# Optimization experiments

Measured on AMD Instinct MI355X. Metric: run time of the kernel, lower is better.

The kernel has to match this reference:

```python
import jax, jax.numpy as jnp
import numpy as np

B, S_ENC, S_DEC, ENC_H, DEC_H = 8, 2048, 2048, 512, 512


def setup_inputs() -> dict:
    key = jax.random.key(0)
    k1, k2, k3 = jax.random.split(key, 3)
    return {
        "enc_hidden_states": jax.random.normal(k1, (B, S_ENC, ENC_H), dtype=jnp.float32),
        "dec_hidden_states": jax.random.normal(k2, (B, S_DEC, DEC_H), dtype=jnp.float32),
        "W_att": jax.random.normal(k3, (ENC_H, DEC_H), dtype=jnp.float32),
    }


def reference(enc_hidden_states, dec_hidden_states, W_att):
    # Project encoder states: [B, S_enc, dec_h]
    enc_proj = jnp.einsum("bse,ed->bsd", enc_hidden_states, W_att)
    # Luong 'general' scores for all decoder timesteps at once: [B, S_dec, S_enc]
    # (original code loops over decoder timesteps via tf.map_fn; this is the
    # equivalent single batched matmul)
    att_logits = jnp.einsum("btd,bsd->bts", dec_hidden_states, enc_proj)
    att_softmax = jax.nn.softmax(att_logits, axis=-1)
    # Attention context vectors: [B, S_dec, enc_h]
    att_vector = jnp.einsum("bts,bse->bte", att_softmax, enc_hidden_states)
    return att_vector
```

## Files before the change

### kernel.cpp

```cpp
#include <hip/hip_runtime.h>
#include <cstdint>


#define DEVINL __device__ __forceinline__

typedef __attribute__((ext_vector_type(8))) short short8;
typedef __attribute__((ext_vector_type(4))) float f32x4;

DEVINL short f2bf(float x) {
    union { float f; uint32_t u; } v; v.f = x;
    uint32_t r = v.u + 0x7FFFu + ((v.u >> 16) & 1u);
    return (short)(r >> 16);
}
DEVINL float bf2f(short h) {
    union { uint32_t u; float f; } v; v.u = ((uint32_t)(uint16_t)h) << 16;
    return v.f;
}

DEVINL void gload_lds16(const void* g, void* l) {
    __builtin_amdgcn_global_load_lds(
        (const __attribute__((address_space(1))) char*)g,
        (__attribute__((address_space(3))) char*)l, 16, 0, 0);
}

__global__ __launch_bounds__(256)
void split_kernel(const float* __restrict__ x, short* __restrict__ hi,
                  short* __restrict__ lo)
{
    long i = ((long)blockIdx.x * 256 + threadIdx.x) * 8;
    f32x4 a = *(const f32x4*)(x + i);
    f32x4 b = *(const f32x4*)(x + i + 4);
    short8 h, l;
#pragma unroll
    for (int j = 0; j < 4; j++) {
        short ha = f2bf(a[j]); h[j] = ha;     l[j] = f2bf(a[j] - bf2f(ha));
        short hb = f2bf(b[j]); h[4 + j] = hb; l[4 + j] = f2bf(b[j] - bf2f(hb));
    }
    *(short8*)(hi + i) = h;
    *(short8*)(lo + i) = l;
}

__global__ __launch_bounds__(256)
void split_w_kernel(const float* __restrict__ w, short* __restrict__ wth,
                    short* __restrict__ wtl)
{
    int idx = blockIdx.x * 256 + threadIdx.x;
    int k = idx >> 9, n = idx & 511;
    float v = w[idx];
    short h = f2bf(v);
    wth[(long)n * 512 + k] = h;
    wtl[(long)n * 512 + k] = f2bf(v - bf2f(h));
}

__global__ __launch_bounds__(256)
void transpose_bf16_kernel(const float* __restrict__ x, short* __restrict__ xt)
{
    __shared__ short tile[32][33];
    const int b  = blockIdx.z;
    const int s0 = blockIdx.x * 32;
    const int e0 = blockIdx.y * 32;
    const float* px = x + (long)b * 2048 * 512;
    short* pt = xt + (long)b * 512 * 2048;
    const int tx = threadIdx.x & 31;
    const int ty = threadIdx.x >> 5;
#pragma unroll
    for (int r = 0; r < 32; r += 8)
        tile[ty + r][tx] = f2bf(px[(long)(s0 + ty + r) * 512 + e0 + tx]);
    __syncthreads();
#pragma unroll
    for (int r = 0; r < 32; r += 8)
        pt[(long)(e0 + ty + r) * 2048 + s0 + tx] = tile[tx][ty + r];
}

template<int NTERMS, bool SPLIT_OUT>
__global__ __launch_bounds__(256, 2)
void gemm_bt(const short* __restrict__ Ah, const short* __restrict__ Al,
             const short* __restrict__ Bh, const short* __restrict__ Bl,
             float* __restrict__ C, short* __restrict__ Ch, short* __restrict__ Cl,
             int K, int lda, int ldb, int ldc,
             long sA, long sB, long sC)
{
    extern __shared__ char smem_raw[];
    constexpr int OPS = (NTERMS == 3) ? 4 : 2;
    constexpr int SET = 128 * 32 * OPS;
    short* smem = (short*)smem_raw;

    const int tid  = threadIdx.x;
    const int wave = tid >> 6;
    const int lane = tid & 63;
    const int quad = lane >> 4;
    const int l16  = lane & 15;
    const int wm   = (wave >> 1) * 64;
    const int wn   = (wave & 1) * 64;

    const long tile_m = (long)blockIdx.y * 128;
    const long tile_n = (long)blockIdx.x * 128;
    const int  bz     = blockIdx.z;

    const short* pAh = Ah + (long)bz * sA;
    const short* pBh = Bh + (long)bz * sB;
    const short* pAl = (NTERMS == 3) ? (Al + (long)bz * sA) : nullptr;
    const short* pBl = (NTERMS == 3) ? (Bl + (long)bz * sB) : nullptr;

    const int srow = tid >> 2;
    const int skq  = (tid & 3) * 8;
    const int lds_off = srow * 32 + skq;
    const long ga0 = (tile_m + srow) * (long)lda + skq;
    const long gb0 = (tile_n + srow) * (long)ldb + skq;

    auto stage = [&](int k0, int buf) {
        short* s   = smem + buf * SET;
        short* ash = s;
        short* bsh = s + 128 * 32;
        gload_lds16(pAh + ga0 + k0,             ash + lds_off);
        gload_lds16(pAh + ga0 + 64l * lda + k0, ash + lds_off + 64 * 32);
        gload_lds16(pBh + gb0 + k0,             bsh + lds_off);
        gload_lds16(pBh + gb0 + 64l * ldb + k0, bsh + lds_off + 64 * 32);
        if constexpr (NTERMS == 3) {
            short* asl = s + 2 * 128 * 32;
            short* bsl = s + 3 * 128 * 32;
            gload_lds16(pAl + ga0 + k0,             asl + lds_off);
            gload_lds16(pAl + ga0 + 64l * lda + k0, asl + lds_off + 64 * 32);
            gload_lds16(pBl + gb0 + k0,             bsl + lds_off);
            gload_lds16(pBl + gb0 + 64l * ldb + k0, bsl + lds_off + 64 * 32);
        }
    };

    f32x4 acc[4][4] = {};
    stage(0, 0);
    int cur = 0;

    for (int k0 = 0; k0 < K; k0 += 32) {
        __syncthreads();
        if (k0 + 32 < K) stage(k0 + 32, cur ^ 1);

        short* s   = smem + cur * SET;
        short* ash = s;
        short* bsh = s + 128 * 32;
        short* asl = s + 2 * 128 * 32;
        short* bsl = s + 3 * 128 * 32;

        short8 ah[4], bh[4], al[4], bl[4];
#pragma unroll
        for (int i = 0; i < 4; i++) {
            ah[i] = *(const short8*)&ash[(wm + i * 16 + l16) * 32 + quad * 8];
            bh[i] = *(const short8*)&bsh[(wn + i * 16 + l16) * 32 + quad * 8];
            if constexpr (NTERMS == 3) {
                al[i] = *(const short8*)&asl[(wm + i * 16 + l16) * 32 + quad * 8];
                bl[i] = *(const short8*)&bsl[(wn + i * 16 + l16) * 32 + quad * 8];
            }
        }
#pragma unroll
        for (int i = 0; i < 4; i++)
#pragma unroll
            for (int j = 0; j < 4; j++) {
                acc[i][j] = __builtin_amdgcn_mfma_f32_16x16x32_bf16(ah[i], bh[j], acc[i][j], 0, 0, 0);
                if constexpr (NTERMS == 3) {
                    acc[i][j] = __builtin_amdgcn_mfma_f32_16x16x32_bf16(ah[i], bl[j], acc[i][j], 0, 0, 0);
                    acc[i][j] = __builtin_amdgcn_mfma_f32_16x16x32_bf16(al[i], bh[j], acc[i][j], 0, 0, 0);
                }
            }
        cur ^= 1;
    }

#pragma unroll
    for (int i = 0; i < 4; i++)
#pragma unroll
        for (int j = 0; j < 4; j++) {
            const long row0 = tile_m + wm + i * 16 + quad * 4;
            const long col  = tile_n + wn + j * 16 + l16;
#pragma unroll
            for (int r = 0; r < 4; r++) {
                float v = acc[i][j][r];
                if constexpr (SPLIT_OUT) {
                    long idx = (long)bz * sC + (row0 + r) * (long)ldc + col;
                    short h = f2bf(v);
                    Ch[idx] = h;
                    Cl[idx] = f2bf(v - bf2f(h));
                } else {
                    C[(long)bz * sC + (row0 + r) * (long)ldc + col] = v;
                }
            }
        }
}

__global__ __launch_bounds__(512, 2)
void gemm3_256(const short* __restrict__ Ah, const short* __restrict__ Al,
               const short* __restrict__ Bh, const short* __restrict__ Bl,
               float* __restrict__ C,
               int K, int lda, int ldb, int ldc,
               long sA, long sB, long sC, int nbx, int nby)
{
    extern __shared__ char smem_raw[];
    short* smem = (short*)smem_raw;
    constexpr int PL  = 256 * 32;
    constexpr int SET = 4 * PL;

    const int t    = threadIdx.x;
    const int wave = t >> 6;
    const int lane = t & 63;
    const int quad = lane >> 4;
    const int l16  = lane & 15;
    const int wm   = (wave >> 2) * 128;
    const int wn   = (wave & 3) * 64;
    const int kslot8 = ((quad ^ ((l16 >> 1) & 3)) << 3);

    const int nwg = gridDim.x;
    const int wg  = blockIdx.x;
    const int swz = (wg & 7) * (nwg >> 3) + (wg >> 3);
    const int per_b = nbx * nby;
    const int bz  = swz / per_b;
    const int rem = swz - bz * per_b;
    const long tile_m = (long)(rem / nbx) * 256;
    const long tile_n = (long)(rem % nbx) * 256;

    const short* pAh = Ah + (long)bz * sA;
    const short* pAl = Al + (long)bz * sA;
    const short* pBh = Bh + (long)bz * sB;
    const short* pBl = Bl + (long)bz * sB;

    const int srow   = t >> 2;
    const int schunk = (t & 3) ^ ((t >> 3) & 3);
    const long gA  = (tile_m + srow) * (long)lda + schunk * 8;
    const long gB  = (tile_n + srow) * (long)ldb + schunk * 8;
    const long gA2 = gA + 128l * lda;
    const long gB2 = gB + 128l * ldb;
    const int ld0 = t * 8;

    f32x4 acc[8][4] = {};

    {
        short* s = smem;
        gload_lds16(pAh + gA,  s + ld0);
        gload_lds16(pAh + gA2, s + ld0 + 4096);
        gload_lds16(pBh + gB,  s + 2 * PL + ld0);
        gload_lds16(pBh + gB2, s + 2 * PL + ld0 + 4096);
        gload_lds16(pAl + gA,  s + PL + ld0);
        gload_lds16(pAl + gA2, s + PL + ld0 + 4096);
        gload_lds16(pBl + gB,  s + 3 * PL + ld0);
        gload_lds16(pBl + gB2, s + 3 * PL + ld0 + 4096);
    }
    asm volatile("s_waitcnt vmcnt(4)" ::: "memory");
    __builtin_amdgcn_s_barrier();

    const int NT = K >> 5;
    int cur = 0;
#pragma unroll 1
    for (int kt = 0; kt < NT; ++kt) {
        const short* s  = smem + cur * SET;
        short* sn       = smem + (cur ^ 1) * SET;
        const short* ah_p = s;
        const short* al_p = s + PL;
        const short* bh_p = s + 2 * PL;
        const short* bl_p = s + 3 * PL;
        const int  k0n  = (kt + 1) << 5;
        const bool more = (kt + 1 < NT);

        short8 xa[8], xb[4];

#pragma unroll
        for (int i = 0; i < 8; i++)
            xa[i] = *(const short8*)&ah_p[(wm + i * 16 + l16) * 32 + kslot8];
#pragma unroll
        for (int j = 0; j < 4; j++)
            xb[j] = *(const short8*)&bh_p[(wn + j * 16 + l16) * 32 + kslot8];
        if (more) {
            gload_lds16(pAh + gA  + k0n, sn + ld0);
            gload_lds16(pAh + gA2 + k0n, sn + ld0 + 4096);
            gload_lds16(pBh + gB  + k0n, sn + 2 * PL + ld0);
            gload_lds16(pBh + gB2 + k0n, sn + 2 * PL + ld0 + 4096);
            asm volatile("s_waitcnt vmcnt(6)" ::: "memory");
        } else {
            asm volatile("s_waitcnt vmcnt(2)" ::: "memory");
        }
        __builtin_amdgcn_s_barrier();
        asm volatile("s_waitcnt lgkmcnt(0)" ::: "memory");
        __builtin_amdgcn_s_setprio(1);
#pragma unroll
        for (int i = 0; i < 8; i++)
#pragma unroll
            for (int j = 0; j < 4; j++)
                acc[i][j] = __builtin_amdgcn_mfma_f32_16x16x32_bf16(xa[i], xb[j], acc[i][j], 0, 0, 0);
        __builtin_amdgcn_s_setprio(0);
        __builtin_amdgcn_s_barrier();

#pragma unroll
        for (int i = 0; i < 8; i++)
            xa[i] = *(const short8*)&al_p[(wm + i * 16 + l16) * 32 + kslot8];
        if (more) {
            gload_lds16(pAl + gA  + k0n, sn + PL + ld0);
            gload_lds16(pAl + gA2 + k0n, sn + PL + ld0 + 4096);
            asm volatile("s_waitcnt vmcnt(6)" ::: "memory");
        } else {
            asm volatile("s_waitcnt vmcnt(0)" ::: "memory");
        }
        __builtin_amdgcn_s_barrier();
        asm volatile("s_waitcnt lgkmcnt(0)" ::: "memory");
        __builtin_amdgcn_s_setprio(1);
#pragma unroll
        for (int i = 0; i < 8; i++)
#pragma unroll
            for (int j = 0; j < 4; j++)
                acc[i][j] = __builtin_amdgcn_mfma_f32_16x16x32_bf16(xa[i], xb[j], acc[i][j], 0, 0, 0);
        __builtin_amdgcn_s_setprio(0);
        __builtin_amdgcn_s_barrier();

#pragma unroll
        for (int j = 0; j < 4; j++)
            xb[j] = *(const short8*)&bl_p[(wn + j * 16 + l16) * 32 + kslot8];
#pragma unroll
        for (int i = 0; i < 8; i++)
            xa[i] = *(const short8*)&ah_p[(wm + i * 16 + l16) * 32 + kslot8];
        if (more) {
            gload_lds16(pBl + gB  + k0n, sn + 3 * PL + ld0);
            gload_lds16(pBl + gB2 + k0n, sn + 3 * PL + ld0 + 4096);
            asm volatile("s_waitcnt vmcnt(4)" ::: "memory");
        }
        __builtin_amdgcn_s_barrier();
        asm volatile("s_waitcnt lgkmcnt(0)" ::: "memory");
        __builtin_amdgcn_s_setprio(1);
#pragma unroll
        for (int i = 0; i < 8; i++)
#pragma unroll
            for (int j = 0; j < 4; j++)
                acc[i][j] = __builtin_amdgcn_mfma_f32_16x16x32_bf16(xa[i], xb[j], acc[i][j], 0, 0, 0);
        __builtin_amdgcn_s_setprio(0);
        __builtin_amdgcn_s_barrier();

        cur ^= 1;
    }

#pragma unroll
    for (int i = 0; i < 8; i++)
#pragma unroll
        for (int j = 0; j < 4; j++) {
            const long row0 = tile_m + wm + i * 16 + quad * 4;
            const long col  = tile_n + wn + j * 16 + l16;
#pragma unroll
            for (int r = 0; r < 4; r++)
                C[(long)bz * sC + (row0 + r) * (long)ldc + col] = acc[i][j][r];
        }
}

__global__ __launch_bounds__(256)
void softmax_kernel(const float* __restrict__ logits, short* __restrict__ P)
{
    const long row = blockIdx.x;
    const float* p = logits + row * 2048;
    const int tid = threadIdx.x;
    const int lane = tid & 63, wave = tid >> 6;

    f32x4 v0 = *(const f32x4*)(p + tid * 8);
    f32x4 v1 = *(const f32x4*)(p + tid * 8 + 4);

    float m = fmaxf(fmaxf(fmaxf(v0[0], v0[1]), fmaxf(v0[2], v0[3])),
                    fmaxf(fmaxf(v1[0], v1[1]), fmaxf(v1[2], v1[3])));
#pragma unroll
    for (int o = 32; o > 0; o >>= 1) m = fmaxf(m, __shfl_xor(m, o));

    __shared__ float red[8];
    if (lane == 0) red[wave] = m;
    __syncthreads();
    m = fmaxf(fmaxf(red[0], red[1]), fmaxf(red[2], red[3]));

    float e[8];
    float s = 0.f;
#pragma unroll
    for (int i = 0; i < 4; i++) { e[i] = __expf(v0[i] - m); s += e[i]; }
#pragma unroll
    for (int i = 0; i < 4; i++) { e[4 + i] = __expf(v1[i] - m); s += e[4 + i]; }
#pragma unroll
    for (int o = 32; o > 0; o >>= 1) s += __shfl_xor(s, o);
    if (lane == 0) red[4 + wave] = s;
    __syncthreads();
    const float inv = 1.f / (red[4] + red[5] + red[6] + red[7]);

    short8 ob;
#pragma unroll
    for (int i = 0; i < 8; i++) ob[i] = f2bf(e[i] * inv);
    *(short8*)(P + row * 2048 + tid * 8) = ob;
}

extern "C" void kernel_launch(void* const* d_in, const int* in_sizes, int n_in,
                              void* d_out, int out_size, void* d_ws, size_t ws_size,
                              hipStream_t stream)
{
    const float* enc = (const float*)d_in[0];
    const float* dec = (const float*)d_in[1];
    const float* W   = (const float*)d_in[2];
    float* out = (float*)d_out;

    const long BSE = 8l * 2048 * 512;
    const long NW  = 512l * 512;

    char* p = (char*)d_ws;
    auto take = [&](long bytes) { char* r = p; p += (bytes + 255) & ~255l; return r; };
    short* enc_hi = (short*)take(BSE * 2);
    short* enc_lo = (short*)take(BSE * 2);
    short* dec_hi = (short*)take(BSE * 2);
    short* dec_lo = (short*)take(BSE * 2);
    short* ep_hi  = (short*)take(BSE * 2);
    short* ep_lo  = (short*)take(BSE * 2);
    short* enc_t  = (short*)take(BSE * 2);
    short* wt_hi  = (short*)take(NW * 2);
    short* wt_lo  = (short*)take(NW * 2);
    float* logits = (float*)take(8l * 2048 * 2048 * 4);
    short* Pbuf = enc_hi;
    (void)ws_size; (void)in_sizes; (void)n_in; (void)out_size;

    static bool attr_set = false;
    if (!attr_set) {
        (void)hipFuncSetAttribute((const void*)gemm3_256,
                                  hipFuncAttributeMaxDynamicSharedMemorySize,
                                  131072);
        attr_set = true;
    }

    split_kernel<<<4096, 256, 0, stream>>>(enc, enc_hi, enc_lo);
    split_kernel<<<4096, 256, 0, stream>>>(dec, dec_hi, dec_lo);
    split_w_kernel<<<1024, 256, 0, stream>>>(W, wt_hi, wt_lo);
    transpose_bf16_kernel<<<dim3(64, 16, 8), 256, 0, stream>>>(enc, enc_t);

    gemm_bt<3, true><<<dim3(4, 128, 1), 256, 64 * 1024, stream>>>(
        enc_hi, enc_lo, wt_hi, wt_lo, nullptr, ep_hi, ep_lo,
        512, 512, 512, 512, 0, 0, 0);

    gemm3_256<<<512, 512, 131072, stream>>>(
        dec_hi, dec_lo, ep_hi, ep_lo, logits,
        512, 512, 512, 2048, 2048l * 512, 2048l * 512, 2048l * 2048, 8, 8);

    softmax_kernel<<<16384, 256, 0, stream>>>(logits, Pbuf);

    gemm_bt<1, false><<<dim3(4, 16, 8), 256, 32 * 1024, stream>>>(
        Pbuf, nullptr, enc_t, nullptr, out, nullptr, nullptr,
        2048, 2048, 2048, 512, 2048l * 2048, 512l * 2048, 2048l * 512);
}
```

Measured before the change: 346.2 us.

## Load B operand directly into registers, stage only A through LDS

After: 370.4 us. 1.07x slower.

```diff
diff --git a/kernel.cpp b/kernel.cpp
--- a/kernel.cpp
+++ b/kernel.cpp
@@ -194,7 +194,7 @@
     extern __shared__ char smem_raw[];
     short* smem = (short*)smem_raw;
     constexpr int PL  = 256 * 32;
-    constexpr int SET = 4 * PL;
+    constexpr int SET = 2 * PL;
 
     const int t    = threadIdx.x;
     const int wave = t >> 6;
@@ -222,111 +222,86 @@
     const int srow   = t >> 2;
     const int schunk = (t & 3) ^ ((t >> 3) & 3);
     const long gA  = (tile_m + srow) * (long)lda + schunk * 8;
-    const long gB  = (tile_n + srow) * (long)ldb + schunk * 8;
     const long gA2 = gA + 128l * lda;
-    const long gB2 = gB + 128l * ldb;
     const int ld0 = t * 8;
 
+    long gb[4];
+#pragma unroll
+    for (int j = 0; j < 4; j++)
+        gb[j] = (tile_n + wn + j * 16 + l16) * (long)ldb + quad * 8;
+
     f32x4 acc[8][4] = {};
+    short8 bh_c[4], bl_c[4];
 
     {
         short* s = smem;
         gload_lds16(pAh + gA,  s + ld0);
         gload_lds16(pAh + gA2, s + ld0 + 4096);
-        gload_lds16(pBh + gB,  s + 2 * PL + ld0);
-        gload_lds16(pBh + gB2, s + 2 * PL + ld0 + 4096);
         gload_lds16(pAl + gA,  s + PL + ld0);
         gload_lds16(pAl + gA2, s + PL + ld0 + 4096);
-        gload_lds16(pBl + gB,  s + 3 * PL + ld0);
-        gload_lds16(pBl + gB2, s + 3 * PL + ld0 + 4096);
     }
-    asm volatile("s_waitcnt vmcnt(4)" ::: "memory");
+    __builtin_amdgcn_sched_barrier(0);
+#pragma unroll
+    for (int j = 0; j < 4; j++) bh_c[j] = *(const short8*)(pBh + gb[j]);
+#pragma unroll
+    for (int j = 0; j < 4; j++) bl_c[j] = *(const short8*)(pBl + gb[j]);
+    asm volatile("s_waitcnt vmcnt(8)" ::: "memory");
     __builtin_amdgcn_s_barrier();
 
     const int NT = K >> 5;
     int cur = 0;
 #pragma unroll 1
     for (int kt = 0; kt < NT; ++kt) {
-        const short* s  = smem + cur * SET;
-        short* sn       = smem + (cur ^ 1) * SET;
+        const short* s    = smem + cur * SET;
         const short* ah_p = s;
         const short* al_p = s + PL;
-        const short* bh_p = s + 2 * PL;
-        const short* bl_p = s + 3 * PL;
-        const int  k0n  = (kt + 1) << 5;
+        const int  k0n = (kt + 1) << 5;
         const bool more = (kt + 1 < NT);
 
-        short8 xa[8], xb[4];
-
-#pragma unroll
-        for (int i = 0; i < 8; i++)
-            xa[i] = *(const short8*)&ah_p[(wm + i * 16 + l16) * 32 + kslot8];
-#pragma unroll
-        for (int j = 0; j < 4; j++)
-            xb[j] = *(const short8*)&bh_p[(wn + j * 16 + l16) * 32 + kslot8];
         if (more) {
+            short* sn = smem + (cur ^ 1) * SET;
             gload_lds16(pAh + gA  + k0n, sn + ld0);
             gload_lds16(pAh + gA2 + k0n, sn + ld0 + 4096);
-            gload_lds16(pBh + gB  + k0n, sn + 2 * PL + ld0);
-            gload_lds16(pBh + gB2 + k0n, sn + 2 * PL + ld0 + 4096);
-            asm volatile("s_waitcnt vmcnt(6)" ::: "memory");
-        } else {
-            asm volatile("s_waitcnt vmcnt(2)" ::: "memory");
-        }
-        __builtin_amdgcn_s_barrier();
-        asm volatile("s_waitcnt lgkmcnt(0)" ::: "memory");
-        __builtin_amdgcn_s_setprio(1);
-#pragma unroll
-        for (int i = 0; i < 8; i++)
-#pragma unroll
-            for (int j = 0; j < 4; j++)
-                acc[i][j] = __builtin_amdgcn_mfma_f32_16x16x32_bf16(xa[i], xb[j], acc[i][j], 0, 0, 0);
-        __builtin_amdgcn_s_setprio(0);
-        __builtin_amdgcn_s_barrier();
-
-#pragma unroll
-        for (int i = 0; i < 8; i++)
-            xa[i] = *(const short8*)&al_p[(wm + i * 16 + l16) * 32 + kslot8];
-        if (more) {
             gload_lds16(pAl + gA  + k0n, sn + PL + ld0);
             gload_lds16(pAl + gA2 + k0n, sn + PL + ld0 + 4096);
-            asm volatile("s_waitcnt vmcnt(6)" ::: "memory");
-        } else {
-            asm volatile("s_waitcnt vmcnt(0)" ::: "memory");
-        }
+        }
+        __builtin_amdgcn_sched_barrier(0);
+
+        short8 xa[8], xl[8];
+#pragma unroll
+        for (int i = 0; i < 8; i++) {
+            xa[i] = *(const short8*)&ah_p[(wm + i * 16 + l16) * 32 + kslot8];
+            xl[i] = *(const short8*)&al_p[(wm + i * 16 + l16) * 32 + kslot8];
+        }
+
+        __builtin_amdgcn_s_setprio(1);
+#pragma unroll
+        for (int i = 0; i < 8; i++)
+#pragma unroll
+            for (int j = 0; j < 4; j++)
+                acc[i][j] = __builtin_amdgcn_mfma_f32_16x16x32_bf16(xa[i], bh_c[j], acc[i][j], 0, 0, 0);
+#pragma unroll
+        for (int i = 0; i < 8; i++)
+#pragma unroll
+            for (int j = 0; j < 4; j++)
+                acc[i][j] = __builtin_amdgcn_mfma_f32_16x16x32_bf16(xl[i], bh_c[j], acc[i][j], 0, 0, 0);
+#pragma unroll
+        for (int i = 0; i < 8; i++)
+#pragma unroll
+            for (int j = 0; j < 4; j++)
+                acc[i][j] = __builtin_amdgcn_mfma_f32_16x16x32_bf16(xa[i], bl_c[j], acc[i][j], 0, 0, 0);
+        __builtin_amdgcn_s_setprio(0);
+
+        if (more) {
+#pragma unroll
+            for (int j = 0; j < 4; j++) bh_c[j] = *(const short8*)(pBh + gb[j] + k0n);
+#pragma unroll
+            for (int j = 0; j < 4; j++) bl_c[j] = *(const short8*)(pBl + gb[j] + k0n);
+        }
+        asm volatile("s_waitcnt lgkmcnt(0)" ::: "memory");
+        if (more)
+            asm volatile("s_waitcnt vmcnt(8)" ::: "memory");
         __builtin_amdgcn_s_barrier();
-        asm volatile("s_waitcnt lgkmcnt(0)" ::: "memory");
-        __builtin_amdgcn_s_setprio(1);
-#pragma unroll
-        for (int i = 0; i < 8; i++)
-#pragma unroll
-            for (int j = 0; j < 4; j++)
-                acc[i][j] = __builtin_amdgcn_mfma_f32_16x16x32_bf16(xa[i], xb[j], acc[i][j], 0, 0, 0);
-        __builtin_amdgcn_s_setprio(0);
-        __builtin_amdgcn_s_barrier();
-
-#pragma unroll
-        for (int j = 0; j < 4; j++)
-            xb[j] = *(const short8*)&bl_p[(wn + j * 16 + l16) * 32 + kslot8];
-#pragma unroll
-        for (int i = 0; i < 8; i++)
-            xa[i] = *(const short8*)&ah_p[(wm + i * 16 + l16) * 32 + kslot8];
-        if (more) {
-            gload_lds16(pBl + gB  + k0n, sn + 3 * PL + ld0);
-            gload_lds16(pBl + gB2 + k0n, sn + 3 * PL + ld0 + 4096);
-            asm volatile("s_waitcnt vmcnt(4)" ::: "memory");
-        }
-        __builtin_amdgcn_s_barrier();
-        asm volatile("s_waitcnt lgkmcnt(0)" ::: "memory");
-        __builtin_amdgcn_s_setprio(1);
-#pragma unroll
-        for (int i = 0; i < 8; i++)
-#pragma unroll
-            for (int j = 0; j < 4; j++)
-                acc[i][j] = __builtin_amdgcn_mfma_f32_16x16x32_bf16(xa[i], xb[j], acc[i][j], 0, 0, 0);
-        __builtin_amdgcn_s_setprio(0);
-        __builtin_amdgcn_s_barrier();
-
         cur ^= 1;
     }
 
@@ -412,7 +387,7 @@
     if (!attr_set) {
         (void)hipFuncSetAttribute((const void*)gemm3_256,
                                   hipFuncAttributeMaxDynamicSharedMemorySize,
-                                  131072);
+                                  65536);
         attr_set = true;
     }
 
@@ -425,7 +400,7 @@
         enc_hi, enc_lo, wt_hi, wt_lo, nullptr, ep_hi, ep_lo,
         512, 512, 512, 512, 0, 0, 0);
 
-    gemm3_256<<<512, 512, 131072, stream>>>(
+    gemm3_256<<<512, 512, 65536, stream>>>(
         dec_hi, dec_lo, ep_hi, ep_lo, logits,
         512, 512, 512, 2048, 2048l * 512, 2048l * 512, 2048l * 2048, 8, 8);
 
```

## Split split-bf16 GEMM main loop into six half-tile MFMA phases

Applied to the files above, without the earlier changes.

Result: slower. 353.9 us (+2.2%).

```diff
diff --git a/kernel.cpp b/kernel.cpp
--- a/kernel.cpp
+++ b/kernel.cpp
@@ -240,15 +240,15 @@
         gload_lds16(pBl + gB,  s + 3 * PL + ld0);
         gload_lds16(pBl + gB2, s + 3 * PL + ld0 + 4096);
     }
-    asm volatile("s_waitcnt vmcnt(4)" ::: "memory");
+    asm volatile("s_waitcnt vmcnt(0)" ::: "memory");
     __builtin_amdgcn_s_barrier();
 
     const int NT = K >> 5;
     int cur = 0;
 #pragma unroll 1
     for (int kt = 0; kt < NT; ++kt) {
-        const short* s  = smem + cur * SET;
-        short* sn       = smem + (cur ^ 1) * SET;
+        const short* s    = smem + cur * SET;
+        short* sn         = smem + (cur ^ 1) * SET;
         const short* ah_p = s;
         const short* al_p = s + PL;
         const short* bh_p = s + 2 * PL;
@@ -256,75 +256,110 @@
         const int  k0n  = (kt + 1) << 5;
         const bool more = (kt + 1 < NT);
 
-        short8 xa[8], xb[4];
-
-#pragma unroll
-        for (int i = 0; i < 8; i++)
-            xa[i] = *(const short8*)&ah_p[(wm + i * 16 + l16) * 32 + kslot8];
+        short8 xah[8], xbh[4], xal[4], xbl[4];
+
+#pragma unroll
+        for (int i = 0; i < 4; i++)
+            xah[i] = *(const short8*)&ah_p[(wm + i * 16 + l16) * 32 + kslot8];
 #pragma unroll
         for (int j = 0; j < 4; j++)
-            xb[j] = *(const short8*)&bh_p[(wn + j * 16 + l16) * 32 + kslot8];
+            xbh[j] = *(const short8*)&bh_p[(wn + j * 16 + l16) * 32 + kslot8];
         if (more) {
             gload_lds16(pAh + gA  + k0n, sn + ld0);
             gload_lds16(pAh + gA2 + k0n, sn + ld0 + 4096);
+        }
+        __builtin_amdgcn_s_barrier();
+        asm volatile("s_waitcnt lgkmcnt(0)" ::: "memory");
+        __builtin_amdgcn_sched_barrier(0);
+        __builtin_amdgcn_s_setprio(1);
+#pragma unroll
+        for (int i = 0; i < 4; i++)
+#pragma unroll
+            for (int j = 0; j < 4; j++)
+                acc[i][j] = __builtin_amdgcn_mfma_f32_16x16x32_bf16(xah[i], xbh[j], acc[i][j], 0, 0, 0);
+        __builtin_amdgcn_s_setprio(0);
+        __builtin_amdgcn_s_barrier();
+
+#pragma unroll
+        for (int i = 4; i < 8; i++)
+            xah[i] = *(const short8*)&ah_p[(wm + i * 16 + l16) * 32 + kslot8];
+        if (more) {
             gload_lds16(pBh + gB  + k0n, sn + 2 * PL + ld0);
             gload_lds16(pBh + gB2 + k0n, sn + 2 * PL + ld0 + 4096);
-            asm volatile("s_waitcnt vmcnt(6)" ::: "memory");
-        } else {
-            asm volatile("s_waitcnt vmcnt(2)" ::: "memory");
         }
         __builtin_amdgcn_s_barrier();
         asm volatile("s_waitcnt lgkmcnt(0)" ::: "memory");
-        __builtin_amdgcn_s_setprio(1);
-#pragma unroll
-        for (int i = 0; i < 8; i++)
-#pragma unroll
-            for (int j = 0; j < 4; j++)
-                acc[i][j] = __builtin_amdgcn_mfma_f32_16x16x32_bf16(xa[i], xb[j], acc[i][j], 0, 0, 0);
-        __builtin_amdgcn_s_setprio(0);
-        __builtin_amdgcn_s_barrier();
-
-#pragma unroll
-        for (int i = 0; i < 8; i++)
-            xa[i] = *(const short8*)&al_p[(wm + i * 16 + l16) * 32 + kslot8];
+        __builtin_amdgcn_sched_barrier(0);
+        __builtin_amdgcn_s_setprio(1);
+#pragma unroll
+        for (int i = 4; i < 8; i++)
+#pragma unroll
+            for (int j = 0; j < 4; j++)
+                acc[i][j] = __builtin_amdgcn_mfma_f32_16x16x32_bf16(xah[i], xbh[j], acc[i][j], 0, 0, 0);
+        __builtin_amdgcn_s_setprio(0);
+        __builtin_amdgcn_s_barrier();
+
+#pragma unroll
+        for (int i = 0; i < 4; i++)
+            xal[i] = *(const short8*)&al_p[(wm + i * 16 + l16) * 32 + kslot8];
         if (more) {
             gload_lds16(pAl + gA  + k0n, sn + PL + ld0);
             gload_lds16(pAl + gA2 + k0n, sn + PL + ld0 + 4096);
-            asm volatile("s_waitcnt vmcnt(6)" ::: "memory");
-        } else {
-            asm volatile("s_waitcnt vmcnt(0)" ::: "memory");
         }
         __builtin_amdgcn_s_barrier();
         asm volatile("s_waitcnt lgkmcnt(0)" ::: "memory");
-        __builtin_amdgcn_s_setprio(1);
-#pragma unroll
-        for (int i = 0; i < 8; i++)
-#pragma unroll
-            for (int j = 0; j < 4; j++)
-                acc[i][j] = __builtin_amdgcn_mfma_f32_16x16x32_bf16(xa[i], xb[j], acc[i][j], 0, 0, 0);
-        __builtin_amdgcn_s_setprio(0);
-        __builtin_amdgcn_s_barrier();
-
-#pragma unroll
-        for (int j = 0; j < 4; j++)
-            xb[j] = *(const short8*)&bl_p[(wn + j * 16 + l16) * 32 + kslot8];
-#pragma unroll
-        for (int i = 0; i < 8; i++)
-            xa[i] = *(const short8*)&ah_p[(wm + i * 16 + l16) * 32 + kslot8];
+        __builtin_amdgcn_sched_barrier(0);
+        __builtin_amdgcn_s_setprio(1);
+#pragma unroll
+        for (int i = 0; i < 4; i++)
+#pragma unroll
+            for (int j = 0; j < 4; j++)
+                acc[i][j] = __builtin_amdgcn_mfma_f32_16x16x32_bf16(xal[i], xbh[j], acc[i][j], 0, 0, 0);
+        __builtin_amdgcn_s_setprio(0);
+        __builtin_amdgcn_s_barrier();
+
+#pragma unroll
+        for (int i = 0; i < 4; i++)
+            xal[i] = *(const short8*)&al_p[(wm + 64 + i * 16 + l16) * 32 + kslot8];
         if (more) {
             gload_lds16(pBl + gB  + k0n, sn + 3 * PL + ld0);
             gload_lds16(pBl + gB2 + k0n, sn + 3 * PL + ld0 + 4096);
-            asm volatile("s_waitcnt vmcnt(4)" ::: "memory");
         }
         __builtin_amdgcn_s_barrier();
         asm volatile("s_waitcnt lgkmcnt(0)" ::: "memory");
-        __builtin_amdgcn_s_setprio(1);
-#pragma unroll
-        for (int i = 0; i < 8; i++)
-#pragma unroll
-            for (int j = 0; j < 4; j++)
-                acc[i][j] = __builtin_amdgcn_mfma_f32_16x16x32_bf16(xa[i], xb[j], acc[i][j], 0, 0, 0);
-        __builtin_amdgcn_s_setprio(0);
+        __builtin_amdgcn_sched_barrier(0);
+        __builtin_amdgcn_s_setprio(1);
+#pragma unroll
+        for (int i = 0; i < 4; i++)
+#pragma unroll
+            for (int j = 0; j < 4; j++)
+                acc[4 + i][j] = __builtin_amdgcn_mfma_f32_16x16x32_bf16(xal[i], xbh[j], acc[4 + i][j], 0, 0, 0);
+        __builtin_amdgcn_s_setprio(0);
+        __builtin_amdgcn_s_barrier();
+
+#pragma unroll
+        for (int j = 0; j < 4; j++)
+            xbl[j] = *(const short8*)&bl_p[(wn + j * 16 + l16) * 32 + kslot8];
+        __builtin_amdgcn_s_barrier();
+        asm volatile("s_waitcnt lgkmcnt(0)" ::: "memory");
+        __builtin_amdgcn_sched_barrier(0);
+        __builtin_amdgcn_s_setprio(1);
+#pragma unroll
+        for (int i = 0; i < 4; i++)
+#pragma unroll
+            for (int j = 0; j < 4; j++)
+                acc[i][j] = __builtin_amdgcn_mfma_f32_16x16x32_bf16(xah[i], xbl[j], acc[i][j], 0, 0, 0);
+        __builtin_amdgcn_s_setprio(0);
+        __builtin_amdgcn_s_barrier();
+
+        __builtin_amdgcn_s_setprio(1);
+#pragma unroll
+        for (int i = 4; i < 8; i++)
+#pragma unroll
+            for (int j = 0; j < 4; j++)
+                acc[i][j] = __builtin_amdgcn_mfma_f32_16x16x32_bf16(xah[i], xbl[j], acc[i][j], 0, 0, 0);
+        __builtin_amdgcn_s_setprio(0);
+        asm volatile("s_waitcnt vmcnt(0)" ::: "memory");
         __builtin_amdgcn_s_barrier();
 
         cur ^= 1;
```
